# Kernel tuning notes

Measured on AMD Instinct MI355X. Metric: run time of the kernel, lower is better.

Reference implementation:

```python
import jax, jax.numpy as jnp
import numpy as np

B, S, D, H = 2, 2048, 1024, 16
HD = D // H  # 64


def setup_inputs() -> dict:
    key = jax.random.key(0)
    ks = jax.random.split(key, 7)
    s = 1.0 / np.sqrt(HD)
    return {
        "x": jax.random.normal(ks[0], (B, S, D), dtype=jnp.float32),
        "Wq": jax.random.normal(ks[1], (H, HD, HD), dtype=jnp.float32) * s,
        "bq": jax.random.normal(ks[2], (H, HD), dtype=jnp.float32) * 0.01,
        "Wk": jax.random.normal(ks[3], (H, HD, HD), dtype=jnp.float32) * s,
        "bk": jax.random.normal(ks[4], (H, HD), dtype=jnp.float32) * 0.01,
        "Wv": jax.random.normal(ks[5], (H, HD, HD), dtype=jnp.float32) * s,
        "bv": jax.random.normal(ks[6], (H, HD), dtype=jnp.float32) * 0.01,
    }


def reference(x, Wq, bq, Wk, bk, Wv, bv):
    b, s, d = x.shape
    h, hd, _ = Wq.shape
    # Faithful to torch: x.view(B, H, S, hd) is a raw reshape (mixes seq positions
    # across heads), NOT a transpose-based head split.
    xh = x.reshape(b, h, s, hd)
    # torch Linear: y @ W.T + b, with W of shape (out, in)
    q = jnp.einsum('bhse,hde->bhsd', xh, Wq) + bq[None, :, None, :]
    k = jnp.einsum('bhse,hde->bhsd', xh, Wk) + bk[None, :, None, :]
    v = jnp.einsum('bhse,hde->bhsd', xh, Wv) + bv[None, :, None, :]
    scale = 1.0 / jnp.sqrt(jnp.asarray(d / h, dtype=jnp.float32))
    attn = jax.nn.softmax(jnp.einsum('bhqd,bhkd->bhqk', q, k) * scale, axis=-1)
    out = jnp.einsum('bhqk,bhkd->bhqd', attn, v)
    # torch.cat over heads along last dim == transpose then merge
    return out.transpose(0, 2, 1, 3).reshape(b, s, d)
```

## Files before the change

### kernel.cpp

```cpp
#include <hip/hip_runtime.h>
#include <hip/hip_bf16.h>

#define BATCH 2
#define SEQ   2048
#define DMODEL 1024
#define NH    16
#define HD    64
#define QSCALE 0.1803368801111602f

typedef __attribute__((ext_vector_type(8))) short bf16x8;
typedef __attribute__((ext_vector_type(4))) float f32x4;

__device__ __forceinline__ ushort f2bf(float f) {
    union { float f; unsigned u; } v; v.f = f;
    return (ushort)((v.u + 0x8000u) >> 16);
}

__device__ __forceinline__ unsigned pack2bf(float a, float b) {
    union { float f; unsigned u; } x, y; x.f = a; y.f = b;
    return __builtin_amdgcn_perm(y.u + 0x8000u, x.u + 0x8000u, 0x07060302u);
}

__device__ __forceinline__ float exp2r(float x) {
#if __has_builtin(__builtin_amdgcn_exp2f)
    return __builtin_amdgcn_exp2f(x);
#else
    return exp2f(x);
#endif
}

__device__ __forceinline__ void g2l16(const void* g, void* l) {
    __builtin_amdgcn_global_load_lds(
        (const __attribute__((address_space(1))) unsigned*)g,
        (__attribute__((address_space(3))) unsigned*)l, 16, 0, 0);
}

#define MFMA(a, b, c) __builtin_amdgcn_mfma_f32_16x16x32_bf16((a), (b), (c), 0, 0, 0)

__global__ __launch_bounds__(256) void qkv_kernel(
    const float* __restrict__ x,
    const float* __restrict__ Wq, const float* __restrict__ bq,
    const float* __restrict__ Wk, const float* __restrict__ bk,
    const float* __restrict__ Wv, const float* __restrict__ bv,
    ushort* __restrict__ Qo, ushort* __restrict__ Kf, ushort* __restrict__ Vf)
{
    const int bid = blockIdx.x;
    const int st  = bid & 31;
    const int bh  = bid >> 5;
    const int h   = bh & (NH - 1);

    __shared__ ushort Xs[64 * 72];
    __shared__ ushort Ws[3 * 64 * 72];

    const int tid  = threadIdx.x;
    const int wave = tid >> 6, lane = tid & 63;
    const int ln16 = lane & 15, quad = lane >> 4;

    const float* wsrc[3] = { Wq + h * 4096, Wk + h * 4096, Wv + h * 4096 };
    for (int m = 0; m < 3; ++m)
        for (int i = 0; i < 4; ++i) {
            int idx = tid + 256 * i;
            float4 v = ((const float4*)wsrc[m])[idx];
            if (m == 0) { v.x *= QSCALE; v.y *= QSCALE; v.z *= QSCALE; v.w *= QSCALE; }
            int row = idx >> 4, c4 = (idx & 15) * 4;
            ushort4 o;
            o.x = f2bf(v.x); o.y = f2bf(v.y); o.z = f2bf(v.z); o.w = f2bf(v.w);
            *(ushort4*)&Ws[m * 64 * 72 + row * 72 + c4] = o;
        }

    const float* xp = x + (size_t)bh * (SEQ * HD) + (size_t)st * 64 * HD;
    for (int i = 0; i < 4; ++i) {
        int idx = tid + 256 * i;
        float4 v = ((const float4*)xp)[idx];
        int row = idx >> 4, c4 = (idx & 15) * 4;
        ushort4 o;
        o.x = f2bf(v.x); o.y = f2bf(v.y); o.z = f2bf(v.z); o.w = f2bf(v.w);
        *(ushort4*)&Xs[row * 72 + c4] = o;
    }
    __syncthreads();

    bf16x8 afr[2];
    for (int ks = 0; ks < 2; ++ks)
        afr[ks] = *(const bf16x8*)&Xs[(wave * 16 + ln16) * 72 + ks * 32 + quad * 8];
    __syncthreads();

    const float* bias[3] = { bq + h * 64, bk + h * 64, bv + h * 64 };
    ushort* Eb = Xs;

    for (int m = 0; m < 3; ++m) {
        f32x4 acc[4];
        for (int nt = 0; nt < 4; ++nt) {
            acc[nt] = (f32x4){0.f, 0.f, 0.f, 0.f};
            for (int ks = 0; ks < 2; ++ks) {
                bf16x8 bfr = *(const bf16x8*)&Ws[m * 64 * 72 + (nt * 16 + ln16) * 72 + ks * 32 + quad * 8];
                acc[nt] = MFMA(afr[ks], bfr, acc[nt]);
            }
        }
        if (m < 2) {
            for (int nt = 0; nt < 4; ++nt) {
                float bb = bias[m][nt * 16 + ln16];
                if (m == 0) bb *= QSCALE;
                for (int r = 0; r < 4; ++r)
                    Eb[(wave * 16 + quad * 4 + r) * 72 + nt * 16 + ln16] = f2bf(acc[nt][r] + bb);
            }
            __syncthreads();
            if (m == 0) {
                ushort* dst = Qo + (size_t)bh * SEQ * HD + (size_t)st * 64 * HD;
                for (int i = 0; i < 2; ++i) {
                    int idx = tid + 256 * i;
                    int row = idx >> 3, c8 = (idx & 7) * 8;
                    *(bf16x8*)&dst[row * 64 + c8] = *(const bf16x8*)&Eb[row * 72 + c8];
                }
            } else {
                ushort* dst = Kf + ((size_t)bh * 32 + st) * 4096;
                for (int i = 0; i < 2; ++i) {
                    int idx8 = tid + 256 * i;
                    int l2 = idx8 & 63, chunk = idx8 >> 6;
                    int nt = chunk >> 1, ks = chunk & 1;
                    int qd = l2 >> 4, l16 = l2 & 15;
                    *(bf16x8*)&dst[(size_t)idx8 * 8] =
                        *(const bf16x8*)&Eb[(nt * 16 + l16) * 72 + ks * 32 + qd * 8];
                }
            }
            __syncthreads();
        } else {
            for (int nt = 0; nt < 4; ++nt) {
                float bb = bias[2][nt * 16 + ln16];
                ushort4 o;
                o.x = f2bf(acc[nt][0] + bb);
                o.y = f2bf(acc[nt][1] + bb);
                o.z = f2bf(acc[nt][2] + bb);
                o.w = f2bf(acc[nt][3] + bb);
                *(ushort4*)&Eb[(nt * 16 + ln16) * 72 + wave * 16 + quad * 4] = o;
            }
            __syncthreads();
            ushort* dst = Vf + ((size_t)bh * 32 + st) * 4096;
            for (int i = 0; i < 2; ++i) {
                int idx8 = tid + 256 * i;
                int l2 = idx8 & 63, chunk = idx8 >> 6;
                int nt = chunk >> 1, ks = chunk & 1;
                int qd = l2 >> 4, l16 = l2 & 15;
                *(bf16x8*)&dst[(size_t)idx8 * 8] =
                    *(const bf16x8*)&Eb[(nt * 16 + l16) * 72 + ks * 32 + qd * 8];
            }
        }
    }
}

__global__ __launch_bounds__(256, 2) void attn_kernel(
    const ushort* __restrict__ Q, const ushort* __restrict__ Kf,
    const ushort* __restrict__ Vf, float* __restrict__ out)
{
    const int bid = blockIdx.x;
    const int wid = (bid & 7) * 64 + (bid >> 3);
    const int qt  = wid & 15;
    const int bh  = wid >> 4;
    const int h   = bh & (NH - 1), b = bh >> 4;

    __shared__ ushort Ksh[2][4096];
    __shared__ ushort Vsh[2][4096];
    __shared__ ushort Ps[4][2][2048];

    const int tid = threadIdx.x, wave = tid >> 6, lane = tid & 63;
    const int ln16 = lane & 15, quad = lane >> 4;
    const unsigned swz = (unsigned)(ln16 & 7) << 4;

    const char* kgb = (const char*)Kf + (size_t)bh * 32 * 8192 + wave * 2048 + lane * 16;
    const char* vgb = (const char*)Vf + (size_t)bh * 32 * 8192 + wave * 2048 + lane * 16;

    auto stage = [&](int kt, int sb) {
        const char* kg = kgb + (size_t)kt * 8192;
        const char* vg = vgb + (size_t)kt * 8192;
        ushort* kl = &Ksh[sb][wave * 1024];
        ushort* vl = &Vsh[sb][wave * 1024];
        g2l16(kg,        kl);
        g2l16(kg + 1024, kl + 512);
        g2l16(vg,        vl);
        g2l16(vg + 1024, vl + 512);
    };

    stage(0, 0);

    bf16x8 qfr[2][2];
#pragma unroll
    for (int g = 0; g < 2; ++g) {
        const ushort* Qg = Q + ((size_t)bh * SEQ + qt * 128 + wave * 32 + g * 16 + ln16) * HD;
        qfr[g][0] = *(const bf16x8*)&Qg[quad * 8];
        qfr[g][1] = *(const bf16x8*)&Qg[32 + quad * 8];
    }

    float lsum[2] = {0.f, 0.f};
    f32x4 accO[2][4];
#pragma unroll
    for (int g = 0; g < 2; ++g)
#pragma unroll
        for (int nt = 0; nt < 4; ++nt) accO[g][nt] = (f32x4){0.f, 0.f, 0.f, 0.f};

    __syncthreads();

    bf16x8 vf[8];

    for (int kt = 0; kt < 32; ++kt) {
        const int cur = kt & 1;

        if (kt < 31) stage(kt + 1, cur ^ 1);

        const ushort* Kb = Ksh[cur];
        bf16x8 kf[8];
#pragma unroll
        for (int c = 0; c < 8; ++c) kf[c] = *(const bf16x8*)&Kb[c * 512 + lane * 8];

        f32x4 sacc[2][4];
#pragma unroll
        for (int nt = 0; nt < 4; ++nt)
#pragma unroll
            for (int g = 0; g < 2; ++g) {
                f32x4 a = {0.f, 0.f, 0.f, 0.f};
                a = MFMA(kf[nt * 2],     qfr[g][0], a);
                a = MFMA(kf[nt * 2 + 1], qfr[g][1], a);
                sacc[g][nt] = a;
            }

        if (kt > 0) {
            const char* Pr = (const char*)Ps[wave][1 - cur];
            bf16x8 pf[2][2];
#pragma unroll
            for (int g = 0; g < 2; ++g) {
                const char* Prr = Pr + (g * 16 + ln16) * 128;
                pf[g][0] = *(const bf16x8*)(Prr + (((unsigned)(quad * 16)) ^ swz));
                pf[g][1] = *(const bf16x8*)(Prr + (((unsigned)(64 + quad * 16)) ^ swz));
            }
#pragma unroll
            for (int nt = 0; nt < 4; ++nt)
#pragma unroll
                for (int g = 0; g < 2; ++g) {
                    accO[g][nt] = MFMA(vf[nt * 2],     pf[g][0], accO[g][nt]);
                    accO[g][nt] = MFMA(vf[nt * 2 + 1], pf[g][1], accO[g][nt]);
                }
        }

        const ushort* Vb = Vsh[cur];
#pragma unroll
        for (int c = 0; c < 8; ++c) vf[c] = *(const bf16x8*)&Vb[c * 512 + lane * 8];

        char* Pw = (char*)Ps[wave][cur];
#pragma unroll
        for (int g = 0; g < 2; ++g) {
            char* Pwr = Pw + (g * 16 + ln16) * 128;
            float rs = 0.f;
#pragma unroll
            for (int nt = 0; nt < 4; ++nt) {
                float p0 = exp2r(sacc[g][nt][0]);
                float p1 = exp2r(sacc[g][nt][1]);
                float p2 = exp2r(sacc[g][nt][2]);
                float p3 = exp2r(sacc[g][nt][3]);
                rs += (p0 + p1) + (p2 + p3);
                uint2 pk;
                pk.x = pack2bf(p0, p1);
                pk.y = pack2bf(p2, p3);
                *(uint2*)(Pwr + (((unsigned)(nt * 32 + quad * 8)) ^ swz)) = pk;
            }
            lsum[g] += rs;
        }

        __syncthreads();
    }

    {
        const char* Pr = (const char*)Ps[wave][1];
        bf16x8 pf[2][2];
#pragma unroll
        for (int g = 0; g < 2; ++g) {
            const char* Prr = Pr + (g * 16 + ln16) * 128;
            pf[g][0] = *(const bf16x8*)(Prr + (((unsigned)(quad * 16)) ^ swz));
            pf[g][1] = *(const bf16x8*)(Prr + (((unsigned)(64 + quad * 16)) ^ swz));
        }
#pragma unroll
        for (int nt = 0; nt < 4; ++nt)
#pragma unroll
            for (int g = 0; g < 2; ++g) {
                accO[g][nt] = MFMA(vf[nt * 2],     pf[g][0], accO[g][nt]);
                accO[g][nt] = MFMA(vf[nt * 2 + 1], pf[g][1], accO[g][nt]);
            }
    }

#pragma unroll
    for (int g = 0; g < 2; ++g) {
        float l = lsum[g];
        l += __shfl_xor(l, 16, 64);
        l += __shfl_xor(l, 32, 64);
        float rinv = 1.0f / l;
        float* ob = out + ((size_t)b * SEQ + qt * 128 + wave * 32 + g * 16 + ln16) * DMODEL + h * HD;
#pragma unroll
        for (int nt = 0; nt < 4; ++nt) {
            float4 o;
            o.x = accO[g][nt][0] * rinv;
            o.y = accO[g][nt][1] * rinv;
            o.z = accO[g][nt][2] * rinv;
            o.w = accO[g][nt][3] * rinv;
            *(float4*)&ob[nt * 16 + quad * 4] = o;
        }
    }
}

extern "C" void kernel_launch(void* const* d_in, const int* in_sizes, int n_in,
                              void* d_out, int out_size, void* d_ws, size_t ws_size,
                              hipStream_t stream) {
    const float* x  = (const float*)d_in[0];
    const float* Wq = (const float*)d_in[1];
    const float* bq = (const float*)d_in[2];
    const float* Wk = (const float*)d_in[3];
    const float* bk = (const float*)d_in[4];
    const float* Wv = (const float*)d_in[5];
    const float* bv = (const float*)d_in[6];

    const size_t nElem = (size_t)BATCH * NH * SEQ * HD;
    ushort* Qw = (ushort*)d_ws;
    ushort* Kw = Qw + nElem;
    ushort* Vw = Kw + nElem;

    qkv_kernel<<<32 * 32, 256, 0, stream>>>(
        x, Wq, bq, Wk, bk, Wv, bv, Qw, Kw, Vw);
    attn_kernel<<<BATCH * NH * (SEQ / 128), 256, 0, stream>>>(
        Qw, Kw, Vw, (float*)d_out);
}
```

Measured before the change: 132.8 us.

## Pre-format weights once, simplify QKV projection, triple-buffer attention K/V loads

Adds a small kernel that converts the per-head Q/K/V weights to bf16 in MFMA fragment order a single time, instead of having every QKV block reload and convert all three matrices through shared memory. The QKV kernel now builds X fragments directly from registers and computes Q, K and V together, using fewer barriers. The attention kernel moves from double to triple buffering of K/V tiles, with explicit vmcnt waits and raw barriers, and adds s_setprio around the MFMA sections so loads have more time to overlap with compute. The costs are an extra kernel launch, more LDS per attention block (which may hurt occupancy at 2 blocks/CU), and hand-written wait counts that must match the number of loads in flight.

Result: no change. 132.5 us (-0.2%).

```diff
diff --git a/kernel.cpp b/kernel.cpp
--- a/kernel.cpp
+++ b/kernel.cpp
@@ -37,11 +37,34 @@
 
 #define MFMA(a, b, c) __builtin_amdgcn_mfma_f32_16x16x32_bf16((a), (b), (c), 0, 0, 0)
 
+__global__ __launch_bounds__(256) void wfmt_kernel(
+    const float* __restrict__ Wq, const float* __restrict__ Wk,
+    const float* __restrict__ Wv, ushort* __restrict__ Wf)
+{
+    const int blk = blockIdx.x;
+    const int h = blk / 3, m = blk - h * 3;
+    const float* W = (m == 0 ? Wq : (m == 1 ? Wk : Wv)) + h * 4096;
+    const float s = (m == 0) ? QSCALE : 1.0f;
+    for (int i = 0; i < 2; ++i) {
+        int idx = threadIdx.x + 256 * i;
+        int l = idx & 63, chunk = idx >> 6;
+        int qd = l >> 4, l16 = l & 15, nt = chunk >> 1, ks = chunk & 1;
+        const float* src = W + (nt * 16 + l16) * 64 + ks * 32 + qd * 8;
+        float4 a = *(const float4*)src;
+        float4 b = *(const float4*)(src + 4);
+        union { bf16x8 v; unsigned u[4]; } t;
+        t.u[0] = pack2bf(a.x * s, a.y * s);
+        t.u[1] = pack2bf(a.z * s, a.w * s);
+        t.u[2] = pack2bf(b.x * s, b.y * s);
+        t.u[3] = pack2bf(b.z * s, b.w * s);
+        *(bf16x8*)&Wf[((size_t)blk * 512 + idx) * 8] = t.v;
+    }
+}
+
 __global__ __launch_bounds__(256) void qkv_kernel(
-    const float* __restrict__ x,
-    const float* __restrict__ Wq, const float* __restrict__ bq,
-    const float* __restrict__ Wk, const float* __restrict__ bk,
-    const float* __restrict__ Wv, const float* __restrict__ bv,
+    const float* __restrict__ x, const ushort* __restrict__ Wf,
+    const float* __restrict__ bq, const float* __restrict__ bk,
+    const float* __restrict__ bv,
     ushort* __restrict__ Qo, ushort* __restrict__ Kf, ushort* __restrict__ Vf)
 {
     const int bid = blockIdx.x;
@@ -49,100 +72,81 @@
     const int bh  = bid >> 5;
     const int h   = bh & (NH - 1);
 
-    __shared__ ushort Xs[64 * 72];
-    __shared__ ushort Ws[3 * 64 * 72];
+    __shared__ ushort EbQ[64 * 72];
+    __shared__ ushort EbK[64 * 72];
+    __shared__ ushort EbV[64 * 72];
 
     const int tid  = threadIdx.x;
     const int wave = tid >> 6, lane = tid & 63;
     const int ln16 = lane & 15, quad = lane >> 4;
 
-    const float* wsrc[3] = { Wq + h * 4096, Wk + h * 4096, Wv + h * 4096 };
+    const float* xr = x + (size_t)bh * (SEQ * HD)
+                        + ((size_t)st * 64 + wave * 16 + ln16) * HD;
+    bf16x8 afr[2];
+#pragma unroll
+    for (int ks = 0; ks < 2; ++ks) {
+        const float4* p = (const float4*)(xr + ks * 32 + quad * 8);
+        float4 a = p[0], b = p[1];
+        union { bf16x8 v; unsigned u[4]; } t;
+        t.u[0] = pack2bf(a.x, a.y);
+        t.u[1] = pack2bf(a.z, a.w);
+        t.u[2] = pack2bf(b.x, b.y);
+        t.u[3] = pack2bf(b.z, b.w);
+        afr[ks] = t.v;
+    }
+
+    const bf16x8* wf = (const bf16x8*)Wf + (size_t)h * 1536 + lane;
+
+    f32x4 acc[3][4];
+#pragma unroll
     for (int m = 0; m < 3; ++m)
-        for (int i = 0; i < 4; ++i) {
+#pragma unroll
+        for (int nt = 0; nt < 4; ++nt) {
+            f32x4 a = {0.f, 0.f, 0.f, 0.f};
+            a = MFMA(afr[0], wf[(m * 8 + nt * 2 + 0) * 64], a);
+            a = MFMA(afr[1], wf[(m * 8 + nt * 2 + 1) * 64], a);
+            acc[m][nt] = a;
+        }
+
+#pragma unroll
+    for (int nt = 0; nt < 4; ++nt) {
+        float bbq = bq[h * 64 + nt * 16 + ln16] * QSCALE;
+        float bbk = bk[h * 64 + nt * 16 + ln16];
+#pragma unroll
+        for (int r = 0; r < 4; ++r) {
+            EbQ[(wave * 16 + quad * 4 + r) * 72 + nt * 16 + ln16] = f2bf(acc[0][nt][r] + bbq);
+            EbK[(wave * 16 + quad * 4 + r) * 72 + nt * 16 + ln16] = f2bf(acc[1][nt][r] + bbk);
+        }
+        float bbv = bv[h * 64 + nt * 16 + ln16];
+        ushort4 o;
+        o.x = f2bf(acc[2][nt][0] + bbv);
+        o.y = f2bf(acc[2][nt][1] + bbv);
+        o.z = f2bf(acc[2][nt][2] + bbv);
+        o.w = f2bf(acc[2][nt][3] + bbv);
+        *(ushort4*)&EbV[(nt * 16 + ln16) * 72 + wave * 16 + quad * 4] = o;
+    }
+    __syncthreads();
+
+    {
+        ushort* dst = Qo + (size_t)bh * SEQ * HD + (size_t)st * 64 * HD;
+        for (int i = 0; i < 2; ++i) {
             int idx = tid + 256 * i;
-            float4 v = ((const float4*)wsrc[m])[idx];
-            if (m == 0) { v.x *= QSCALE; v.y *= QSCALE; v.z *= QSCALE; v.w *= QSCALE; }
-            int row = idx >> 4, c4 = (idx & 15) * 4;
-            ushort4 o;
-            o.x = f2bf(v.x); o.y = f2bf(v.y); o.z = f2bf(v.z); o.w = f2bf(v.w);
-            *(ushort4*)&Ws[m * 64 * 72 + row * 72 + c4] = o;
-        }
-
-    const float* xp = x + (size_t)bh * (SEQ * HD) + (size_t)st * 64 * HD;
-    for (int i = 0; i < 4; ++i) {
-        int idx = tid + 256 * i;
-        float4 v = ((const float4*)xp)[idx];
-        int row = idx >> 4, c4 = (idx & 15) * 4;
-        ushort4 o;
-        o.x = f2bf(v.x); o.y = f2bf(v.y); o.z = f2bf(v.z); o.w = f2bf(v.w);
-        *(ushort4*)&Xs[row * 72 + c4] = o;
-    }
-    __syncthreads();
-
-    bf16x8 afr[2];
-    for (int ks = 0; ks < 2; ++ks)
-        afr[ks] = *(const bf16x8*)&Xs[(wave * 16 + ln16) * 72 + ks * 32 + quad * 8];
-    __syncthreads();
-
-    const float* bias[3] = { bq + h * 64, bk + h * 64, bv + h * 64 };
-    ushort* Eb = Xs;
-
-    for (int m = 0; m < 3; ++m) {
-        f32x4 acc[4];
-        for (int nt = 0; nt < 4; ++nt) {
-            acc[nt] = (f32x4){0.f, 0.f, 0.f, 0.f};
-            for (int ks = 0; ks < 2; ++ks) {
-                bf16x8 bfr = *(const bf16x8*)&Ws[m * 64 * 72 + (nt * 16 + ln16) * 72 + ks * 32 + quad * 8];
-                acc[nt] = MFMA(afr[ks], bfr, acc[nt]);
-            }
-        }
-        if (m < 2) {
-            for (int nt = 0; nt < 4; ++nt) {
-                float bb = bias[m][nt * 16 + ln16];
-                if (m == 0) bb *= QSCALE;
-                for (int r = 0; r < 4; ++r)
-                    Eb[(wave * 16 + quad * 4 + r) * 72 + nt * 16 + ln16] = f2bf(acc[nt][r] + bb);
-            }
-            __syncthreads();
-            if (m == 0) {
-                ushort* dst = Qo + (size_t)bh * SEQ * HD + (size_t)st * 64 * HD;
-                for (int i = 0; i < 2; ++i) {
-                    int idx = tid + 256 * i;
-                    int row = idx >> 3, c8 = (idx & 7) * 8;
-                    *(bf16x8*)&dst[row * 64 + c8] = *(const bf16x8*)&Eb[row * 72 + c8];
-                }
-            } else {
-                ushort* dst = Kf + ((size_t)bh * 32 + st) * 4096;
-                for (int i = 0; i < 2; ++i) {
-                    int idx8 = tid + 256 * i;
-                    int l2 = idx8 & 63, chunk = idx8 >> 6;
-                    int nt = chunk >> 1, ks = chunk & 1;
-                    int qd = l2 >> 4, l16 = l2 & 15;
-                    *(bf16x8*)&dst[(size_t)idx8 * 8] =
-                        *(const bf16x8*)&Eb[(nt * 16 + l16) * 72 + ks * 32 + qd * 8];
-                }
-            }
-            __syncthreads();
-        } else {
-            for (int nt = 0; nt < 4; ++nt) {
-                float bb = bias[2][nt * 16 + ln16];
-                ushort4 o;
-                o.x = f2bf(acc[nt][0] + bb);
-                o.y = f2bf(acc[nt][1] + bb);
-                o.z = f2bf(acc[nt][2] + bb);
-                o.w = f2bf(acc[nt][3] + bb);
-                *(ushort4*)&Eb[(nt * 16 + ln16) * 72 + wave * 16 + quad * 4] = o;
-            }
-            __syncthreads();
-            ushort* dst = Vf + ((size_t)bh * 32 + st) * 4096;
-            for (int i = 0; i < 2; ++i) {
-                int idx8 = tid + 256 * i;
-                int l2 = idx8 & 63, chunk = idx8 >> 6;
-                int nt = chunk >> 1, ks = chunk & 1;
-                int qd = l2 >> 4, l16 = l2 & 15;
-                *(bf16x8*)&dst[(size_t)idx8 * 8] =
-                    *(const bf16x8*)&Eb[(nt * 16 + l16) * 72 + ks * 32 + qd * 8];
-            }
+            int row = idx >> 3, c8 = (idx & 7) * 8;
+            *(bf16x8*)&dst[row * 64 + c8] = *(const bf16x8*)&EbQ[row * 72 + c8];
+        }
+    }
+    {
+        ushort* dstK = Kf + ((size_t)bh * 32 + st) * 4096;
+        ushort* dstV = Vf + ((size_t)bh * 32 + st) * 4096;
+        for (int i = 0; i < 2; ++i) {
+            int idx8 = tid + 256 * i;
+            int l2 = idx8 & 63, chunk = idx8 >> 6;
+            int nt = chunk >> 1, ks = chunk & 1;
+            int qd = l2 >> 4, l16 = l2 & 15;
+            *(bf16x8*)&dstK[(size_t)idx8 * 8] =
+                *(const bf16x8*)&EbK[(nt * 16 + l16) * 72 + ks * 32 + qd * 8];
+            *(bf16x8*)&dstV[(size_t)idx8 * 8] =
+                *(const bf16x8*)&EbV[(nt * 16 + l16) * 72 + ks * 32 + qd * 8];
         }
     }
 }
@@ -157,8 +161,8 @@
     const int bh  = wid >> 4;
     const int h   = bh & (NH - 1), b = bh >> 4;
 
-    __shared__ ushort Ksh[2][4096];
-    __shared__ ushort Vsh[2][4096];
+    __shared__ ushort Ksh[3][4096];
+    __shared__ ushort Vsh[3][4096];
     __shared__ ushort Ps[4][2][2048];
 
     const int tid = threadIdx.x, wave = tid >> 6, lane = tid & 63;
@@ -180,6 +184,7 @@
     };
 
     stage(0, 0);
+    stage(1, 1);
 
     bf16x8 qfr[2][2];
 #pragma unroll
@@ -196,21 +201,27 @@
 #pragma unroll
         for (int nt = 0; nt < 4; ++nt) accO[g][nt] = (f32x4){0.f, 0.f, 0.f, 0.f};
 
-    __syncthreads();
-
     bf16x8 vf[8];
 
     for (int kt = 0; kt < 32; ++kt) {
         const int cur = kt & 1;
-
-        if (kt < 31) stage(kt + 1, cur ^ 1);
-
-        const ushort* Kb = Ksh[cur];
+        const int sb  = kt % 3;
+
+        if (kt < 31) {
+            asm volatile("s_waitcnt vmcnt(4)" ::: "memory");
+        } else {
+            asm volatile("s_waitcnt vmcnt(0)" ::: "memory");
+        }
+        __builtin_amdgcn_s_barrier();
+        __builtin_amdgcn_sched_barrier(0);
+
+        const ushort* Kb = &Ksh[sb][0];
         bf16x8 kf[8];
 #pragma unroll
         for (int c = 0; c < 8; ++c) kf[c] = *(const bf16x8*)&Kb[c * 512 + lane * 8];
 
         f32x4 sacc[2][4];
+        __builtin_amdgcn_s_setprio(1);
 #pragma unroll
         for (int nt = 0; nt < 4; ++nt)
 #pragma unroll
@@ -220,6 +231,7 @@
                 a = MFMA(kf[nt * 2 + 1], qfr[g][1], a);
                 sacc[g][nt] = a;
             }
+        __builtin_amdgcn_s_setprio(0);
 
         if (kt > 0) {
             const char* Pr = (const char*)Ps[wave][1 - cur];
@@ -230,6 +242,7 @@
                 pf[g][0] = *(const bf16x8*)(Prr + (((unsigned)(quad * 16)) ^ swz));
                 pf[g][1] = *(const bf16x8*)(Prr + (((unsigned)(64 + quad * 16)) ^ swz));
             }
+            __builtin_amdgcn_s_setprio(1);
 #pragma unroll
             for (int nt = 0; nt < 4; ++nt)
 #pragma unroll
@@ -237,9 +250,10 @@
                     accO[g][nt] = MFMA(vf[nt * 2],     pf[g][0], accO[g][nt]);
                     accO[g][nt] = MFMA(vf[nt * 2 + 1], pf[g][1], accO[g][nt]);
                 }
-        }
-
-        const ushort* Vb = Vsh[cur];
+            __builtin_amdgcn_s_setprio(0);
+        }
+
+        const ushort* Vb = &Vsh[sb][0];
 #pragma unroll
         for (int c = 0; c < 8; ++c) vf[c] = *(const bf16x8*)&Vb[c * 512 + lane * 8];
 
@@ -263,7 +277,11 @@
             lsum[g] += rs;
         }
 
-        __syncthreads();
+        if (kt < 30) {
+            asm volatile("s_waitcnt lgkmcnt(0)" ::: "memory");
+            __builtin_amdgcn_sched_barrier(0);
+            stage(kt + 2, (kt + 2) % 3);
+        }
     }
 
     {
@@ -315,12 +333,14 @@
     const float* bv = (const float*)d_in[6];
 
     const size_t nElem = (size_t)BATCH * NH * SEQ * HD;
-    ushort* Qw = (ushort*)d_ws;
-    ushort* Kw = Qw + nElem;
-    ushort* Vw = Kw + nElem;
-
+    ushort* Qw  = (ushort*)d_ws;
+    ushort* Kw  = Qw + nElem;
+    ushort* Vw  = Kw + nElem;
+    ushort* Wfw = Vw + nElem;
+
+    wfmt_kernel<<<48, 256, 0, stream>>>(Wq, Wk, Wv, Wfw);
     qkv_kernel<<<32 * 32, 256, 0, stream>>>(
-        x, Wq, bq, Wk, bk, Wv, bv, Qw, Kw, Vw);
+        x, Wfw, bq, bk, bv, Qw, Kw, Vw);
     attn_kernel<<<BATCH * NH * (SEQ / 128), 256, 0, stream>>>(
         Qw, Kw, Vw, (float*)d_out);
 }
```
